# Performance work log

Hardware: AMD Instinct MI355X
Metric: run time of the kernel (lower is better)

Reference implementation:

```python
import jax, jax.numpy as jnp
import numpy as np

N, E, D, H = 100000, 1600000, 128, 4
HD = D // H  # per-head dim


def setup_inputs() -> dict:
    key = jax.random.key(0)
    ks = jax.random.split(key, 16)
    s = 1.0 / np.sqrt(D)
    inp = {
        "x": jax.random.normal(ks[0], (N, D), jnp.float32),
        "edge_index": jax.random.randint(ks[1], (2, E), 0, N, jnp.int64),
        # GCNConv params
        "w_gcn": jax.random.normal(ks[2], (D, D), jnp.float32) * s,
        "b_gcn": jnp.zeros((D,), jnp.float32),
        # TransformerConv params (lin_query/key/value, lin_skip, lin_beta)
        "w_q": jax.random.normal(ks[3], (D, D), jnp.float32) * s,
        "b_q": jnp.zeros((D,), jnp.float32),
        "w_k": jax.random.normal(ks[4], (D, D), jnp.float32) * s,
        "b_k": jnp.zeros((D,), jnp.float32),
        "w_v": jax.random.normal(ks[5], (D, D), jnp.float32) * s,
        "b_v": jnp.zeros((D,), jnp.float32),
        "w_skip": jax.random.normal(ks[6], (D, D), jnp.float32) * s,
        "b_skip": jnp.zeros((D,), jnp.float32),
        "w_beta": jax.random.normal(ks[7], (3 * D, 1), jnp.float32) * s,
        # LayerNorms
        "ln1_g": jnp.ones((D,), jnp.float32),
        "ln1_b": jnp.zeros((D,), jnp.float32),
        "ln2_g": jnp.ones((D,), jnp.float32),
        "ln2_b": jnp.zeros((D,), jnp.float32),
        # FFN
        "w1": jax.random.normal(ks[8], (D, 2 * D), jnp.float32) * s,
        "b1": jnp.zeros((2 * D,), jnp.float32),
        "w2": jax.random.normal(ks[9], (2 * D, D), jnp.float32) * (1.0 / np.sqrt(2 * D)),
        "b2": jnp.zeros((D,), jnp.float32),
        "local_weight": jnp.ones((1,), jnp.float32),
        "global_weight": jnp.ones((1,), jnp.float32),
    }
    return inp


def _layer_norm(x, g, b, eps=1e-5):
    mu = jnp.mean(x, axis=-1, keepdims=True)
    var = jnp.var(x, axis=-1, keepdims=True)
    return (x - mu) * jax.lax.rsqrt(var + eps) * g + b


def _gps_forward(x, edge_index, w_gcn, b_gcn, w_q, b_q, w_k, b_k, w_v, b_v,
                 w_skip, b_skip, w_beta, ln1_g, ln1_b, ln2_g, ln2_b,
                 w1, b1, w2, b2, local_weight, global_weight):
    src, dst = edge_index[0], edge_index[1]  # messages flow src -> dst

    # ---- GCNConv (add_self_loops=False), sym norm ----
    deg = jax.ops.segment_sum(jnp.ones((E,), x.dtype), dst, num_segments=N)
    dinv = jnp.where(deg > 0, jax.lax.rsqrt(jnp.maximum(deg, 1.0)), 0.0)
    norm = dinv[src] * dinv[dst]  # [E]
    h = x @ w_gcn  # [N, D]
    local_out = jax.ops.segment_sum(h[src] * norm[:, None], dst, num_segments=N) + b_gcn

    # ---- TransformerConv (heads=H, concat=True, beta=True) ----
    q = (x @ w_q + b_q).reshape(N, H, HD)
    k = (x @ w_k + b_k).reshape(N, H, HD)
    v = (x @ w_v + b_v).reshape(N, H, HD)
    scores = jnp.sum(q[dst] * k[src], axis=-1) / np.sqrt(HD)  # [E, H]
    m = jax.ops.segment_max(scores, dst, num_segments=N)      # [N, H]
    m = jnp.where(jnp.isfinite(m), m, 0.0)
    e = jnp.exp(scores - m[dst])                              # [E, H]
    denom = jax.ops.segment_sum(e, dst, num_segments=N)       # [N, H]
    alpha = e / denom[dst]                                    # [E, H]
    agg = jax.ops.segment_sum(v[src] * alpha[:, :, None], dst, num_segments=N)
    out_attn = agg.reshape(N, D)
    x_r = x @ w_skip + b_skip
    beta = jax.nn.sigmoid(
        jnp.concatenate([out_attn, x_r, out_attn - x_r], axis=-1) @ w_beta)  # [N,1]
    global_out = beta * x_r + (1.0 - beta) * out_attn

    # ---- combine + LN + FFN + LN ----
    xc = local_weight * local_out + global_weight * global_out
    xn = _layer_norm(xc + xc, ln1_g, ln1_b)
    ff = jnp.maximum(xn @ w1 + b1, 0.0) @ w2 + b2
    return _layer_norm(ff + xn, ln2_g, ln2_b)


def reference(x, edge_index, w_gcn, b_gcn, w_q, b_q, w_k, b_k, w_v, b_v,
              w_skip, b_skip, w_beta, ln1_g, ln1_b, ln2_g, ln2_b,
              w1, b1, w2, b2, local_weight, global_weight):
    return _gps_forward(x, edge_index, w_gcn, b_gcn, w_q, b_q, w_k, b_k, w_v, b_v,
                        w_skip, b_skip, w_beta, ln1_g, ln1_b, ln2_g, ln2_b,
                        w1, b1, w2, b2, local_weight, global_weight)
```

## Files before the change

kernel.cpp:

```cpp
#include <hip/hip_runtime.h>

typedef unsigned int u32;
typedef unsigned short u16;
typedef __attribute__((ext_vector_type(8))) short bf16x8;
typedef __attribute__((ext_vector_type(4))) float f32x4;

__device__ __forceinline__ float bf2f(u16 u){ return __uint_as_float(((u32)u) << 16); }
__device__ __forceinline__ float bf2f_lo(u32 u){ return __uint_as_float(u << 16); }
__device__ __forceinline__ float bf2f_hi(u32 u){ return __uint_as_float(u & 0xffff0000u); }
__device__ __forceinline__ u16 f2bf(float f){
  u32 x = __float_as_uint(f);
  return (u16)((x + 0x7fffu + ((x >> 16) & 1u)) >> 16);
}

__global__ void k_prep_all(const float* wq, const float* bq, const float* wsk, const float* bsk,
                           const float* wk, const float* bk, const float* wv, const float* bv,
                           const float* wg, const float* w1, const float* w2,
                           u16* WcatT, float* bcat, u16* w1T, u16* w2T){
  int idx = blockIdx.x * 256 + threadIdx.x;
  if (idx < 640 * 128){
    int col = idx >> 7, k = idx & 127;
    int blk = col >> 7, c = col & 127;
    const float* w = (blk==0)?wq:(blk==1)?wsk:(blk==2)?wk:(blk==3)?wv:wg;
    WcatT[idx] = f2bf(w[k * 128 + c]);
    if (k == 0){
      const float* b = (blk==0)?bq:(blk==1)?bsk:(blk==2)?bk:(blk==3)?bv:nullptr;
      bcat[col] = b ? b[c] : 0.0f;
    }
  } else if (idx < 640*128 + 256*128){
    int j = idx - 640*128; int c = j >> 7, k = j & 127;
    w1T[j] = f2bf(w1[k * 256 + c]);
  } else if (idx < 640*128 + 256*128 + 128*256){
    int j = idx - (640*128 + 256*128); int c = j >> 8, k = j & 255;
    w2T[j] = f2bf(w2[k * 128 + c]);
  }
}

__global__ void k_hist(const int* __restrict__ ei, int E, int* __restrict__ deg){
  int e = blockIdx.x * 256 + threadIdx.x;
  if (e >= E) return;
  atomicAdd(&deg[ei[E + e]], 1);
}
__global__ void k_scan_a(const int* __restrict__ deg, int N, int* __restrict__ bsum){
  __shared__ int sh[256];
  int b = blockIdx.x, t = threadIdx.x;
  int base = b * 1024 + t * 4, s = 0;
  #pragma unroll
  for (int j = 0; j < 4; j++){ int i = base + j; if (i < N) s += deg[i]; }
  sh[t] = s; __syncthreads();
  for (int off = 128; off > 0; off >>= 1){ if (t < off) sh[t] += sh[t + off]; __syncthreads(); }
  if (t == 0) bsum[b] = sh[0];
}
__global__ void k_scan_b(const int* __restrict__ bsum, int NB, int* __restrict__ boff){
  __shared__ int sh[1024];
  int t = threadIdx.x;
  int self = (t < NB) ? bsum[t] : 0;
  sh[t] = self; __syncthreads();
  for (int off = 1; off < 1024; off <<= 1){
    int v = sh[t]; int add = (t >= off) ? sh[t - off] : 0;
    __syncthreads(); sh[t] = v + add; __syncthreads();
  }
  if (t < NB) boff[t] = sh[t] - self;
}
__global__ void k_scan_c(const int* __restrict__ deg, int N, int E,
                         const int* __restrict__ boff, int* __restrict__ rowptr,
                         float* __restrict__ dinv){
  __shared__ int sh[256];
  int b = blockIdx.x, t = threadIdx.x;
  int base = b * 1024 + t * 4;
  int d[4]; int ts = 0;
  #pragma unroll
  for (int j = 0; j < 4; j++){ int i = base + j; d[j] = (i < N) ? deg[i] : 0; ts += d[j]; }
  sh[t] = ts; __syncthreads();
  for (int off = 1; off < 256; off <<= 1){
    int v = sh[t]; int add = (t >= off) ? sh[t - off] : 0;
    __syncthreads(); sh[t] = v + add; __syncthreads();
  }
  int excl = sh[t] - ts + boff[b];
  #pragma unroll
  for (int j = 0; j < 4; j++){
    int i = base + j;
    if (i < N){
      rowptr[i] = excl;
      dinv[i] = d[j] > 0 ? rsqrtf((float)d[j]) : 0.0f;
    }
    excl += d[j];
  }
  if (b == 0 && t == 0) rowptr[N] = E;
}
__global__ void k_csr(const int* __restrict__ ei, int E,
                      const int* __restrict__ rowptr, int* __restrict__ fill, int* __restrict__ csr){
  int e = blockIdx.x * 256 + threadIdx.x;
  if (e >= E) return;
  int d = ei[E + e];
  int pos = rowptr[d] + atomicAdd(&fill[d], 1);
  csr[pos] = ei[e];
}

__device__ __forceinline__ void stageTile(const u16* __restrict__ g, int ldg, int row0, int rclamp,
                                          int kofs, u16* lds){
  int t = threadIdx.x;
  #pragma unroll
  for (int p = 0; p < 8; p++){
    int chunk = p * 256 + t;
    int r = chunk >> 4;
    int cs = (chunk & 15) << 3;
    int rg = row0 + r; if (rg >= rclamp) rg = rclamp - 1;
    bf16x8 v = *(const bf16x8*)(g + (size_t)rg * ldg + kofs + cs);
    *(bf16x8*)(lds + r * 128 + (cs ^ ((r & 7) << 3))) = v;
  }
}
__device__ __forceinline__ void stageTileF32(const float* __restrict__ g, int ldg, int row0,
                                             int rclamp, u16* lds){
  int t = threadIdx.x;
  #pragma unroll
  for (int p = 0; p < 8; p++){
    int chunk = p * 256 + t;
    int r = chunk >> 4;
    int cs = (chunk & 15) << 3;
    int rg = row0 + r; if (rg >= rclamp) rg = rclamp - 1;
    const float* src = g + (size_t)rg * ldg + cs;
    float4 a = *(const float4*)(src);
    float4 b = *(const float4*)(src + 4);
    u16* dst = lds + r * 128 + (cs ^ ((r & 7) << 3));
    ushort4 lo; lo.x = f2bf(a.x); lo.y = f2bf(a.y); lo.z = f2bf(a.z); lo.w = f2bf(a.w);
    ushort4 hi; hi.x = f2bf(b.x); hi.y = f2bf(b.y); hi.z = f2bf(b.z); hi.w = f2bf(b.w);
    *(ushort4*)dst = lo;
    *(ushort4*)(dst + 4) = hi;
  }
}
__device__ __forceinline__ bf16x8 ldFrag(const u16* lds, int r, int k0){
  return *(const bf16x8*)(lds + r * 128 + (k0 ^ ((r & 7) << 3)));
}

__global__ __launch_bounds__(256) void k_gemm1(const float* __restrict__ x, const u16* __restrict__ WcatT,
    const float* __restrict__ bcat, u16* __restrict__ qB, u16* __restrict__ xrB,
    u16* __restrict__ kvhB, int N){
  __shared__ u16 As[128 * 128];
  __shared__ u16 Bs[128 * 128];
  int row0 = blockIdx.x * 128;
  stageTileF32(x, 128, row0, N, As);
  int t = threadIdx.x, l = t & 63, w = t >> 6;
  int wm = w >> 1, wn = w & 1;
  int c16 = l & 15, g = l >> 4;
  for (int cb = 0; cb < 5; cb++){
    stageTile(WcatT, 128, cb * 128, 1 << 30, 0, Bs);
    __syncthreads();
    f32x4 acc[4][4];
    #pragma unroll
    for (int mi = 0; mi < 4; mi++)
      #pragma unroll
      for (int ni = 0; ni < 4; ni++) acc[mi][ni] = (f32x4){0.f, 0.f, 0.f, 0.f};
    #pragma unroll
    for (int kk = 0; kk < 4; kk++){
      int k0 = kk * 32 + g * 8;
      bf16x8 af[4], bfr[4];
      #pragma unroll
      for (int mi = 0; mi < 4; mi++) af[mi] = ldFrag(As, wm * 64 + mi * 16 + c16, k0);
      #pragma unroll
      for (int ni = 0; ni < 4; ni++) bfr[ni] = ldFrag(Bs, wn * 64 + ni * 16 + c16, k0);
      #pragma unroll
      for (int mi = 0; mi < 4; mi++)
        #pragma unroll
        for (int ni = 0; ni < 4; ni++)
          acc[mi][ni] = __builtin_amdgcn_mfma_f32_16x16x32_bf16(af[mi], bfr[ni], acc[mi][ni], 0, 0, 0);
    }
    u16* dst; int ld, cofs;
    if (cb == 0){ dst = qB;  ld = 128; cofs = 0; }
    else if (cb == 1){ dst = xrB; ld = 128; cofs = 0; }
    else { dst = kvhB; ld = 384; cofs = (cb - 2) * 128; }
    float bias[4];
    #pragma unroll
    for (int ni = 0; ni < 4; ni++) bias[ni] = bcat[cb * 128 + wn * 64 + ni * 16 + c16];
    #pragma unroll
    for (int mi = 0; mi < 4; mi++){
      #pragma unroll
      for (int r = 0; r < 4; r++){
        int row = row0 + wm * 64 + mi * 16 + g * 4 + r;
        if (row < N){
          #pragma unroll
          for (int ni = 0; ni < 4; ni++)
            dst[(size_t)row * ld + cofs + wn * 64 + ni * 16 + c16] = f2bf(acc[mi][ni][r] + bias[ni]);
        }
      }
    }
    __syncthreads();
  }
}

__global__ __launch_bounds__(256) void k_edge(const u16* __restrict__ qB, const u16* __restrict__ xrB,
    const u16* __restrict__ kvhB,
    const int* __restrict__ csr, const int* __restrict__ rowptr, const float* __restrict__ dinv,
    const float* __restrict__ bgcn, const float* __restrict__ wbeta,
    const float* __restrict__ lng, const float* __restrict__ lnb,
    const float* __restrict__ lwp, const float* __restrict__ gwp,
    u16* __restrict__ xnB, int N){
  int lane = threadIdx.x & 63;
  int half = lane >> 5;
  int li = lane & 31;
  int d0 = li * 4;
  int n = blockIdx.x * 4 + (threadIdx.x >> 6);
  if (n >= N) return;
  int ro = rowptr[n], re = rowptr[n + 1];
  uint2 qu = *(const uint2*)(qB + (size_t)n * 128 + d0);
  float q0 = bf2f_lo(qu.x), q1 = bf2f_hi(qu.x), q2 = bf2f_lo(qu.y), q3 = bf2f_hi(qu.y);
  float av0 = 0, av1 = 0, av2 = 0, av3 = 0;
  float ah0 = 0, ah1 = 0, ah2 = 0, ah3 = 0;
  float den = 0;
  const float SC = 0.17677669529663687f;
  for (int e = ro + half; e < re; e += 2){
    int s = csr[e];
    const u16* fb = kvhB + (size_t)s * 384;
    uint2 ku = *(const uint2*)(fb + d0);
    uint2 vu = *(const uint2*)(fb + 128 + d0);
    uint2 hu = *(const uint2*)(fb + 256 + d0);
    float dv = dinv[s];
    float part = q0 * bf2f_lo(ku.x) + q1 * bf2f_hi(ku.x)
               + q2 * bf2f_lo(ku.y) + q3 * bf2f_hi(ku.y);
    part += __shfl_xor(part, 1);
    part += __shfl_xor(part, 2);
    part += __shfl_xor(part, 4);
    float p = __expf(part * SC);
    av0 += p * bf2f_lo(vu.x); av1 += p * bf2f_hi(vu.x);
    av2 += p * bf2f_lo(vu.y); av3 += p * bf2f_hi(vu.y);
    ah0 += dv * bf2f_lo(hu.x); ah1 += dv * bf2f_hi(hu.x);
    ah2 += dv * bf2f_lo(hu.y); ah3 += dv * bf2f_hi(hu.y);
    den += p;
  }
  den += __shfl_xor(den, 32);
  av0 += __shfl_xor(av0, 32); av1 += __shfl_xor(av1, 32);
  av2 += __shfl_xor(av2, 32); av3 += __shfl_xor(av3, 32);
  ah0 += __shfl_xor(ah0, 32); ah1 += __shfl_xor(ah1, 32);
  ah2 += __shfl_xor(ah2, 32); ah3 += __shfl_xor(ah3, 32);
  float inv_den = den > 0 ? 1.0f / den : 0.0f;
  float at0 = av0 * inv_den, at1 = av1 * inv_den, at2 = av2 * inv_den, at3 = av3 * inv_den;
  uint2 xru = *(const uint2*)(xrB + (size_t)n * 128 + d0);
  float xr0 = bf2f_lo(xru.x), xr1 = bf2f_hi(xru.x), xr2 = bf2f_lo(xru.y), xr3 = bf2f_hi(xru.y);
  float4 wb0 = *(const float4*)(wbeta + d0);
  float4 wb1 = *(const float4*)(wbeta + 128 + d0);
  float4 wb2 = *(const float4*)(wbeta + 256 + d0);
  float z = at0 * wb0.x + at1 * wb0.y + at2 * wb0.z + at3 * wb0.w
          + xr0 * wb1.x + xr1 * wb1.y + xr2 * wb1.z + xr3 * wb1.w
          + (at0 - xr0) * wb2.x + (at1 - xr1) * wb2.y
          + (at2 - xr2) * wb2.z + (at3 - xr3) * wb2.w;
  z += __shfl_xor(z, 1); z += __shfl_xor(z, 2); z += __shfl_xor(z, 4);
  z += __shfl_xor(z, 8); z += __shfl_xor(z, 16);
  float beta = 1.0f / (1.0f + __expf(-z));
  float dn = dinv[n];
  float4 bg = *(const float4*)(bgcn + d0);
  float l0 = dn * ah0 + bg.x, l1 = dn * ah1 + bg.y, l2 = dn * ah2 + bg.z, l3 = dn * ah3 + bg.w;
  float lw = lwp[0], gw = gwp[0];
  float ib = 1.0f - beta;
  float t0 = 2.0f * (lw * l0 + gw * (beta * xr0 + ib * at0));
  float t1 = 2.0f * (lw * l1 + gw * (beta * xr1 + ib * at1));
  float t2 = 2.0f * (lw * l2 + gw * (beta * xr2 + ib * at2));
  float t3 = 2.0f * (lw * l3 + gw * (beta * xr3 + ib * at3));
  float s = t0 + t1 + t2 + t3;
  float sq = t0*t0 + t1*t1 + t2*t2 + t3*t3;
  s += __shfl_xor(s, 1);  sq += __shfl_xor(sq, 1);
  s += __shfl_xor(s, 2);  sq += __shfl_xor(sq, 2);
  s += __shfl_xor(s, 4);  sq += __shfl_xor(sq, 4);
  s += __shfl_xor(s, 8);  sq += __shfl_xor(sq, 8);
  s += __shfl_xor(s, 16); sq += __shfl_xor(sq, 16);
  float mu = s * (1.0f / 128.0f);
  float var = sq * (1.0f / 128.0f) - mu * mu;
  float inv = rsqrtf(var + 1e-5f);
  if (half == 0){
    float4 gm = *(const float4*)(lng + d0);
    float4 bt = *(const float4*)(lnb + d0);
    float o0 = (t0 - mu) * inv * gm.x + bt.x;
    float o1 = (t1 - mu) * inv * gm.y + bt.y;
    float o2 = (t2 - mu) * inv * gm.z + bt.z;
    float o3 = (t3 - mu) * inv * gm.w + bt.w;
    uint2 pk;
    pk.x = (u32)f2bf(o0) | ((u32)f2bf(o1) << 16);
    pk.y = (u32)f2bf(o2) | ((u32)f2bf(o3) << 16);
    *(uint2*)(xnB + (size_t)n * 128 + d0) = pk;
  }
}

__global__ __launch_bounds__(256) void k_ffn1(const u16* __restrict__ xnB, const u16* __restrict__ w1T,
    const float* __restrict__ b1, u16* __restrict__ hid, int N){
  __shared__ u16 As[128 * 128];
  __shared__ u16 Bs[128 * 128];
  int row0 = blockIdx.x * 128, cb = blockIdx.y;
  stageTile(xnB, 128, row0, N, 0, As);
  stageTile(w1T, 128, cb * 128, 1 << 30, 0, Bs);
  __syncthreads();
  int t = threadIdx.x, l = t & 63, w = t >> 6;
  int wm = w >> 1, wn = w & 1;
  int c16 = l & 15, g = l >> 4;
  f32x4 acc[4][4];
  #pragma unroll
  for (int mi = 0; mi < 4; mi++)
    #pragma unroll
    for (int ni = 0; ni < 4; ni++) acc[mi][ni] = (f32x4){0.f, 0.f, 0.f, 0.f};
  #pragma unroll
  for (int kk = 0; kk < 4; kk++){
    int k0 = kk * 32 + g * 8;
    bf16x8 af[4], bfr[4];
    #pragma unroll
    for (int mi = 0; mi < 4; mi++) af[mi] = ldFrag(As, wm * 64 + mi * 16 + c16, k0);
    #pragma unroll
    for (int ni = 0; ni < 4; ni++) bfr[ni] = ldFrag(Bs, wn * 64 + ni * 16 + c16, k0);
    #pragma unroll
    for (int mi = 0; mi < 4; mi++)
      #pragma unroll
      for (int ni = 0; ni < 4; ni++)
        acc[mi][ni] = __builtin_amdgcn_mfma_f32_16x16x32_bf16(af[mi], bfr[ni], acc[mi][ni], 0, 0, 0);
  }
  float bias[4];
  #pragma unroll
  for (int ni = 0; ni < 4; ni++) bias[ni] = b1[cb * 128 + wn * 64 + ni * 16 + c16];
  #pragma unroll
  for (int mi = 0; mi < 4; mi++){
    #pragma unroll
    for (int r = 0; r < 4; r++){
      int row = row0 + wm * 64 + mi * 16 + g * 4 + r;
      if (row < N){
        #pragma unroll
        for (int ni = 0; ni < 4; ni++)
          hid[(size_t)row * 256 + cb * 128 + wn * 64 + ni * 16 + c16] =
              f2bf(fmaxf(acc[mi][ni][r] + bias[ni], 0.0f));
      }
    }
  }
}

__global__ __launch_bounds__(256) void k_ffn2(const u16* __restrict__ hid, const u16* __restrict__ w2T,
    const float* __restrict__ b2, const u16* __restrict__ xnB,
    const float* __restrict__ g2, const float* __restrict__ bt2,
    float* __restrict__ out, int N){
  __shared__ u16 As[128 * 128];
  __shared__ u16 Bs[128 * 128];
  int row0 = blockIdx.x * 128;
  int t = threadIdx.x, l = t & 63, w = t >> 6;
  int c16 = l & 15, g = l >> 4;
  f32x4 acc[2][8];
  #pragma unroll
  for (int mi = 0; mi < 2; mi++)
    #pragma unroll
    for (int ni = 0; ni < 8; ni++) acc[mi][ni] = (f32x4){0.f, 0.f, 0.f, 0.f};
  for (int kc = 0; kc < 2; kc++){
    if (kc) __syncthreads();
    stageTile(hid, 256, row0, N, kc * 128, As);
    stageTile(w2T, 256, 0, 1 << 30, kc * 128, Bs);
    __syncthreads();
    #pragma unroll
    for (int kk = 0; kk < 4; kk++){
      int k0 = kk * 32 + g * 8;
      bf16x8 af[2], bfr[8];
      #pragma unroll
      for (int mi = 0; mi < 2; mi++) af[mi] = ldFrag(As, w * 32 + mi * 16 + c16, k0);
      #pragma unroll
      for (int ni = 0; ni < 8; ni++) bfr[ni] = ldFrag(Bs, ni * 16 + c16, k0);
      #pragma unroll
      for (int mi = 0; mi < 2; mi++)
        #pragma unroll
        for (int ni = 0; ni < 8; ni++)
          acc[mi][ni] = __builtin_amdgcn_mfma_f32_16x16x32_bf16(af[mi], bfr[ni], acc[mi][ni], 0, 0, 0);
    }
  }
  float b2c[8], g2c[8], btc[8];
  #pragma unroll
  for (int ni = 0; ni < 8; ni++){
    int col = ni * 16 + c16;
    b2c[ni] = b2[col]; g2c[ni] = g2[col]; btc[ni] = bt2[col];
  }
  #pragma unroll
  for (int mi = 0; mi < 2; mi++){
    #pragma unroll
    for (int r = 0; r < 4; r++){
      int row = row0 + w * 32 + mi * 16 + g * 4 + r;
      int rc = row < N ? row : N - 1;
      float z[8]; float s = 0.f, sq = 0.f;
      #pragma unroll
      for (int ni = 0; ni < 8; ni++){
        float xv = bf2f(xnB[(size_t)rc * 128 + ni * 16 + c16]);
        z[ni] = acc[mi][ni][r] + b2c[ni] + xv;
        s += z[ni]; sq += z[ni] * z[ni];
      }
      s += __shfl_xor(s, 1); sq += __shfl_xor(sq, 1);
      s += __shfl_xor(s, 2); sq += __shfl_xor(sq, 2);
      s += __shfl_xor(s, 4); sq += __shfl_xor(sq, 4);
      s += __shfl_xor(s, 8); sq += __shfl_xor(sq, 8);
      float mu = s * (1.0f / 128.0f);
      float var = sq * (1.0f / 128.0f) - mu * mu;
      float inv = rsqrtf(var + 1e-5f);
      if (row < N){
        #pragma unroll
        for (int ni = 0; ni < 8; ni++)
          out[(size_t)row * 128 + ni * 16 + c16] = (z[ni] - mu) * inv * g2c[ni] + btc[ni];
      }
    }
  }
}

extern "C" void kernel_launch(void* const* d_in, const int* in_sizes, int n_in,
                              void* d_out, int out_size, void* d_ws, size_t ws_size,
                              hipStream_t stream){
  const float* x      = (const float*)d_in[0];
  const int*   ei     = (const int*)d_in[1];
  const float* w_gcn  = (const float*)d_in[2];
  const float* b_gcn  = (const float*)d_in[3];
  const float* w_q    = (const float*)d_in[4];
  const float* b_q    = (const float*)d_in[5];
  const float* w_k    = (const float*)d_in[6];
  const float* b_k    = (const float*)d_in[7];
  const float* w_v    = (const float*)d_in[8];
  const float* b_v    = (const float*)d_in[9];
  const float* w_skip = (const float*)d_in[10];
  const float* b_skip = (const float*)d_in[11];
  const float* w_beta = (const float*)d_in[12];
  const float* ln1_g  = (const float*)d_in[13];
  const float* ln1_b  = (const float*)d_in[14];
  const float* ln2_g  = (const float*)d_in[15];
  const float* ln2_b  = (const float*)d_in[16];
  const float* w1     = (const float*)d_in[17];
  const float* b1     = (const float*)d_in[18];
  const float* w2     = (const float*)d_in[19];
  const float* b2     = (const float*)d_in[20];
  const float* lw     = (const float*)d_in[21];
  const float* gw     = (const float*)d_in[22];
  int N = in_sizes[0] / 128;
  int E = in_sizes[1] / 2;
  float* outf = (float*)d_out;

  char* ws = (char*)d_ws;
  size_t off = 0;
  auto alloc = [&](size_t bytes) -> char* {
    char* p = ws + off; off += (bytes + 255) & ~(size_t)255; return p;
  };
  u16* kvhB   = (u16*)alloc((size_t)N * 384 * 2);
  u16* xrB    = (u16*)alloc((size_t)N * 128 * 2);
  u16* qB     = (u16*)alloc((size_t)N * 128 * 2);
  u16* xnB    = (u16*)alloc((size_t)N * 128 * 2);
  int* csr    = (int*)alloc((size_t)E * 4);
  int* deg    = (int*)alloc((size_t)N * 4);
  int* rowptr = (int*)alloc((size_t)(N + 1) * 4);
  int* fill   = (int*)alloc((size_t)N * 4);
  float* dinv = (float*)alloc((size_t)N * 4);
  int NB = (N + 1023) >> 10;
  int* bsum   = (int*)alloc((size_t)NB * 4);
  int* boff   = (int*)alloc((size_t)NB * 4);
  u16* WcatT  = (u16*)alloc((size_t)640 * 128 * 2);
  float* bcat = (float*)alloc((size_t)640 * 4);
  u16* w1T    = (u16*)alloc((size_t)256 * 128 * 2);
  u16* w2T    = (u16*)alloc((size_t)128 * 256 * 2);
  u16* hid    = kvhB;

  if (off > ws_size) return;

  hipMemsetAsync(deg, 0, (size_t)N * 4, stream);
  hipMemsetAsync(fill, 0, (size_t)N * 4, stream);

  k_prep_all<<<576, 256, 0, stream>>>(w_q, b_q, w_skip, b_skip, w_k, b_k, w_v, b_v, w_gcn,
                                      w1, w2, WcatT, bcat, w1T, w2T);
  k_hist<<<(E + 255) / 256, 256, 0, stream>>>(ei, E, deg);
  k_scan_a<<<NB, 256, 0, stream>>>(deg, N, bsum);
  k_scan_b<<<1, 1024, 0, stream>>>(bsum, NB, boff);
  k_scan_c<<<NB, 256, 0, stream>>>(deg, N, E, boff, rowptr, dinv);
  k_csr<<<(E + 255) / 256, 256, 0, stream>>>(ei, E, rowptr, fill, csr);

  int MB = (N + 127) / 128;
  k_gemm1<<<MB, 256, 0, stream>>>(x, WcatT, bcat, qB, xrB, kvhB, N);
  k_edge<<<(N + 3) / 4, 256, 0, stream>>>(qB, xrB, kvhB, csr, rowptr, dinv, b_gcn, w_beta,
                                          ln1_g, ln1_b, lw, gw, xnB, N);
  dim3 f1(MB, 2);
  k_ffn1<<<f1, 256, 0, stream>>>(xnB, w1T, b1, hid, N);
  k_ffn2<<<MB, 256, 0, stream>>>(hid, w2T, b2, xnB, ln2_g, ln2_b, outf, N);
}
```

Baseline: 455.3 us.

## Fuse FFN kernels via LDS hidden tile, prescale GCN features by dinv, reuse deg for CSR fill

Merges the two FFN GEMM kernels into one that keeps the 64x256 ReLU hidden tile in shared memory, so the hidden activations no longer make a round trip through global memory. The GCN source-side dinv scaling moves into the first GEMM epilogue, which removes a per-edge dinv gather in the edge kernel. CSR construction now decrements the degree array instead of incrementing a separate zeroed fill array, dropping one memset and one buffer. The fused FFN uses 64 KB of LDS per block with smaller row tiles, which may lower occupancy and reload the weights once per 64 rows.

```diff
diff --git a/kernel.cpp b/kernel.cpp
--- a/kernel.cpp
+++ b/kernel.cpp
@@ -89,11 +89,11 @@
   if (b == 0 && t == 0) rowptr[N] = E;
 }
 __global__ void k_csr(const int* __restrict__ ei, int E,
-                      const int* __restrict__ rowptr, int* __restrict__ fill, int* __restrict__ csr){
+                      const int* __restrict__ rowptr, int* __restrict__ deg, int* __restrict__ csr){
   int e = blockIdx.x * 256 + threadIdx.x;
   if (e >= E) return;
   int d = ei[E + e];
-  int pos = rowptr[d] + atomicAdd(&fill[d], 1);
+  int pos = rowptr[d] + atomicSub(&deg[d], 1) - 1;
   csr[pos] = ei[e];
 }
 
@@ -134,8 +134,8 @@
 }
 
 __global__ __launch_bounds__(256) void k_gemm1(const float* __restrict__ x, const u16* __restrict__ WcatT,
-    const float* __restrict__ bcat, u16* __restrict__ qB, u16* __restrict__ xrB,
-    u16* __restrict__ kvhB, int N){
+    const float* __restrict__ bcat, const float* __restrict__ dinv,
+    u16* __restrict__ qB, u16* __restrict__ xrB, u16* __restrict__ kvhB, int N){
   __shared__ u16 As[128 * 128];
   __shared__ u16 Bs[128 * 128];
   int row0 = blockIdx.x * 128;
@@ -165,10 +165,6 @@
         for (int ni = 0; ni < 4; ni++)
           acc[mi][ni] = __builtin_amdgcn_mfma_f32_16x16x32_bf16(af[mi], bfr[ni], acc[mi][ni], 0, 0, 0);
     }
-    u16* dst; int ld, cofs;
-    if (cb == 0){ dst = qB;  ld = 128; cofs = 0; }
-    else if (cb == 1){ dst = xrB; ld = 128; cofs = 0; }
-    else { dst = kvhB; ld = 384; cofs = (cb - 2) * 128; }
     float bias[4];
     #pragma unroll
     for (int ni = 0; ni < 4; ni++) bias[ni] = bcat[cb * 128 + wn * 64 + ni * 16 + c16];
@@ -178,9 +174,23 @@
       for (int r = 0; r < 4; r++){
         int row = row0 + wm * 64 + mi * 16 + g * 4 + r;
         if (row < N){
-          #pragma unroll
-          for (int ni = 0; ni < 4; ni++)
-            dst[(size_t)row * ld + cofs + wn * 64 + ni * 16 + c16] = f2bf(acc[mi][ni][r] + bias[ni]);
+          if (cb == 0 || cb == 1){
+            u16* dst = (cb == 0 ? qB : xrB) + (size_t)row * 128;
+            #pragma unroll
+            for (int ni = 0; ni < 4; ni++)
+              dst[wn * 64 + ni * 16 + c16] = f2bf(acc[mi][ni][r] + bias[ni]);
+          } else if (cb == 4){
+            float dv = dinv[row];
+            u16* dst = kvhB + (size_t)row * 384 + 256;
+            #pragma unroll
+            for (int ni = 0; ni < 4; ni++)
+              dst[wn * 64 + ni * 16 + c16] = f2bf(acc[mi][ni][r] * dv);
+          } else {
+            u16* dst = kvhB + (size_t)row * 384 + (cb - 2) * 128;
+            #pragma unroll
+            for (int ni = 0; ni < 4; ni++)
+              dst[wn * 64 + ni * 16 + c16] = f2bf(acc[mi][ni][r] + bias[ni]);
+          }
         }
       }
     }
@@ -214,7 +224,6 @@
     uint2 ku = *(const uint2*)(fb + d0);
     uint2 vu = *(const uint2*)(fb + 128 + d0);
     uint2 hu = *(const uint2*)(fb + 256 + d0);
-    float dv = dinv[s];
     float part = q0 * bf2f_lo(ku.x) + q1 * bf2f_hi(ku.x)
                + q2 * bf2f_lo(ku.y) + q3 * bf2f_hi(ku.y);
     part += __shfl_xor(part, 1);
@@ -223,8 +232,8 @@
     float p = __expf(part * SC);
     av0 += p * bf2f_lo(vu.x); av1 += p * bf2f_hi(vu.x);
     av2 += p * bf2f_lo(vu.y); av3 += p * bf2f_hi(vu.y);
-    ah0 += dv * bf2f_lo(hu.x); ah1 += dv * bf2f_hi(hu.x);
-    ah2 += dv * bf2f_lo(hu.y); ah3 += dv * bf2f_hi(hu.y);
+    ah0 += bf2f_lo(hu.x); ah1 += bf2f_hi(hu.x);
+    ah2 += bf2f_lo(hu.y); ah3 += bf2f_hi(hu.y);
     den += p;
   }
   den += __shfl_xor(den, 32);
@@ -279,87 +288,86 @@
   }
 }
 
-__global__ __launch_bounds__(256) void k_ffn1(const u16* __restrict__ xnB, const u16* __restrict__ w1T,
-    const float* __restrict__ b1, u16* __restrict__ hid, int N){
-  __shared__ u16 As[128 * 128];
-  __shared__ u16 Bs[128 * 128];
-  int row0 = blockIdx.x * 128, cb = blockIdx.y;
-  stageTile(xnB, 128, row0, N, 0, As);
-  stageTile(w1T, 128, cb * 128, 1 << 30, 0, Bs);
-  __syncthreads();
-  int t = threadIdx.x, l = t & 63, w = t >> 6;
-  int wm = w >> 1, wn = w & 1;
-  int c16 = l & 15, g = l >> 4;
-  f32x4 acc[4][4];
-  #pragma unroll
-  for (int mi = 0; mi < 4; mi++)
-    #pragma unroll
-    for (int ni = 0; ni < 4; ni++) acc[mi][ni] = (f32x4){0.f, 0.f, 0.f, 0.f};
-  #pragma unroll
-  for (int kk = 0; kk < 4; kk++){
-    int k0 = kk * 32 + g * 8;
-    bf16x8 af[4], bfr[4];
-    #pragma unroll
-    for (int mi = 0; mi < 4; mi++) af[mi] = ldFrag(As, wm * 64 + mi * 16 + c16, k0);
-    #pragma unroll
-    for (int ni = 0; ni < 4; ni++) bfr[ni] = ldFrag(Bs, wn * 64 + ni * 16 + c16, k0);
-    #pragma unroll
-    for (int mi = 0; mi < 4; mi++)
-      #pragma unroll
-      for (int ni = 0; ni < 4; ni++)
-        acc[mi][ni] = __builtin_amdgcn_mfma_f32_16x16x32_bf16(af[mi], bfr[ni], acc[mi][ni], 0, 0, 0);
-  }
-  float bias[4];
-  #pragma unroll
-  for (int ni = 0; ni < 4; ni++) bias[ni] = b1[cb * 128 + wn * 64 + ni * 16 + c16];
-  #pragma unroll
-  for (int mi = 0; mi < 4; mi++){
-    #pragma unroll
-    for (int r = 0; r < 4; r++){
-      int row = row0 + wm * 64 + mi * 16 + g * 4 + r;
-      if (row < N){
-        #pragma unroll
-        for (int ni = 0; ni < 4; ni++)
-          hid[(size_t)row * 256 + cb * 128 + wn * 64 + ni * 16 + c16] =
-              f2bf(fmaxf(acc[mi][ni][r] + bias[ni], 0.0f));
-      }
-    }
-  }
-}
-
-__global__ __launch_bounds__(256) void k_ffn2(const u16* __restrict__ hid, const u16* __restrict__ w2T,
-    const float* __restrict__ b2, const u16* __restrict__ xnB,
+__global__ __launch_bounds__(256) void k_ffn(const u16* __restrict__ xnB, const u16* __restrict__ w1T,
+    const float* __restrict__ b1, const u16* __restrict__ w2T, const float* __restrict__ b2,
     const float* __restrict__ g2, const float* __restrict__ bt2,
     float* __restrict__ out, int N){
-  __shared__ u16 As[128 * 128];
-  __shared__ u16 Bs[128 * 128];
-  int row0 = blockIdx.x * 128;
+  __shared__ u16 L[32768];
+  int row0 = blockIdx.x * 64;
   int t = threadIdx.x, l = t & 63, w = t >> 6;
   int c16 = l & 15, g = l >> 4;
-  f32x4 acc[2][8];
-  #pragma unroll
-  for (int mi = 0; mi < 2; mi++)
-    #pragma unroll
-    for (int ni = 0; ni < 8; ni++) acc[mi][ni] = (f32x4){0.f, 0.f, 0.f, 0.f};
-  for (int kc = 0; kc < 2; kc++){
-    if (kc) __syncthreads();
-    stageTile(hid, 256, row0, N, kc * 128, As);
-    stageTile(w2T, 256, 0, 1 << 30, kc * 128, Bs);
+  #pragma unroll
+  for (int p = 0; p < 4; p++){
+    int chunk = p * 256 + t;
+    int r = chunk >> 4, cs = (chunk & 15) << 3;
+    int rg = row0 + r; if (rg >= N) rg = N - 1;
+    bf16x8 v = *(const bf16x8*)(xnB + (size_t)rg * 128 + cs);
+    *(bf16x8*)(L + r * 128 + (cs ^ ((r & 7) << 3))) = v;
+  }
+  f32x4 acc1[2][8];
+  #pragma unroll
+  for (int cb = 0; cb < 2; cb++)
+    #pragma unroll
+    for (int ni = 0; ni < 8; ni++) acc1[cb][ni] = (f32x4){0.f, 0.f, 0.f, 0.f};
+  for (int cb = 0; cb < 2; cb++){
+    #pragma unroll
+    for (int p = 0; p < 8; p++){
+      int chunk = p * 256 + t;
+      int r = chunk >> 4, cs = (chunk & 15) << 3;
+      bf16x8 v = *(const bf16x8*)(w1T + (size_t)(cb * 128 + r) * 128 + cs);
+      *(bf16x8*)(L + 8192 + r * 128 + (cs ^ ((r & 7) << 3))) = v;
+    }
     __syncthreads();
     #pragma unroll
     for (int kk = 0; kk < 4; kk++){
       int k0 = kk * 32 + g * 8;
-      bf16x8 af[2], bfr[8];
-      #pragma unroll
-      for (int mi = 0; mi < 2; mi++) af[mi] = ldFrag(As, w * 32 + mi * 16 + c16, k0);
-      #pragma unroll
-      for (int ni = 0; ni < 8; ni++) bfr[ni] = ldFrag(Bs, ni * 16 + c16, k0);
-      #pragma unroll
-      for (int mi = 0; mi < 2; mi++)
-        #pragma unroll
-        for (int ni = 0; ni < 8; ni++)
-          acc[mi][ni] = __builtin_amdgcn_mfma_f32_16x16x32_bf16(af[mi], bfr[ni], acc[mi][ni], 0, 0, 0);
-    }
+      bf16x8 af = ldFrag(L, w * 16 + c16, k0);
+      #pragma unroll
+      for (int ni = 0; ni < 8; ni++){
+        bf16x8 bfr = ldFrag(L + 8192, ni * 16 + c16, k0);
+        acc1[cb][ni] = __builtin_amdgcn_mfma_f32_16x16x32_bf16(af, bfr, acc1[cb][ni], 0, 0, 0);
+      }
+    }
+    __syncthreads();
+  }
+  #pragma unroll
+  for (int cb = 0; cb < 2; cb++){
+    #pragma unroll
+    for (int ni = 0; ni < 8; ni++){
+      float bias = b1[cb * 128 + ni * 16 + c16];
+      #pragma unroll
+      for (int r = 0; r < 4; r++){
+        int rl = w * 16 + g * 4 + r;
+        int col = cb * 128 + ni * 16 + c16;
+        L[rl * 256 + (col ^ ((rl & 7) << 3))] = f2bf(fmaxf(acc1[cb][ni][r] + bias, 0.f));
+      }
+    }
+  }
+  __syncthreads();
+  f32x4 acc2[8];
+  #pragma unroll
+  for (int ni = 0; ni < 8; ni++) acc2[ni] = (f32x4){0.f, 0.f, 0.f, 0.f};
+  for (int kc = 0; kc < 2; kc++){
+    #pragma unroll
+    for (int p = 0; p < 8; p++){
+      int chunk = p * 256 + t;
+      int r = chunk >> 4, cs = (chunk & 15) << 3;
+      bf16x8 v = *(const bf16x8*)(w2T + (size_t)r * 256 + kc * 128 + cs);
+      *(bf16x8*)(L + 16384 + r * 128 + (cs ^ ((r & 7) << 3))) = v;
+    }
+    __syncthreads();
+    #pragma unroll
+    for (int kk = 0; kk < 4; kk++){
+      int k0 = kk * 32 + g * 8;
+      int rowl = w * 16 + c16;
+      bf16x8 af = *(const bf16x8*)(L + rowl * 256 + ((kc * 128 + k0) ^ ((rowl & 7) << 3)));
+      #pragma unroll
+      for (int ni = 0; ni < 8; ni++){
+        bf16x8 bfr = ldFrag(L + 16384, ni * 16 + c16, k0);
+        acc2[ni] = __builtin_amdgcn_mfma_f32_16x16x32_bf16(af, bfr, acc2[ni], 0, 0, 0);
+      }
+    }
+    __syncthreads();
   }
   float b2c[8], g2c[8], btc[8];
   #pragma unroll
@@ -368,30 +376,27 @@
     b2c[ni] = b2[col]; g2c[ni] = g2[col]; btc[ni] = bt2[col];
   }
   #pragma unroll
-  for (int mi = 0; mi < 2; mi++){
-    #pragma unroll
-    for (int r = 0; r < 4; r++){
-      int row = row0 + w * 32 + mi * 16 + g * 4 + r;
-      int rc = row < N ? row : N - 1;
-      float z[8]; float s = 0.f, sq = 0.f;
-      #pragma unroll
-      for (int ni = 0; ni < 8; ni++){
-        float xv = bf2f(xnB[(size_t)rc * 128 + ni * 16 + c16]);
-        z[ni] = acc[mi][ni][r] + b2c[ni] + xv;
-        s += z[ni]; sq += z[ni] * z[ni];
-      }
-      s += __shfl_xor(s, 1); sq += __shfl_xor(sq, 1);
-      s += __shfl_xor(s, 2); sq += __shfl_xor(sq, 2);
-      s += __shfl_xor(s, 4); sq += __shfl_xor(sq, 4);
-      s += __shfl_xor(s, 8); sq += __shfl_xor(sq, 8);
-      float mu = s * (1.0f / 128.0f);
-      float var = sq * (1.0f / 128.0f) - mu * mu;
-      float inv = rsqrtf(var + 1e-5f);
-      if (row < N){
-        #pragma unroll
-        for (int ni = 0; ni < 8; ni++)
-          out[(size_t)row * 128 + ni * 16 + c16] = (z[ni] - mu) * inv * g2c[ni] + btc[ni];
-      }
+  for (int r = 0; r < 4; r++){
+    int row = row0 + w * 16 + g * 4 + r;
+    int rc = row < N ? row : N - 1;
+    float z[8]; float s = 0.f, sq = 0.f;
+    #pragma unroll
+    for (int ni = 0; ni < 8; ni++){
+      float xv = bf2f(xnB[(size_t)rc * 128 + ni * 16 + c16]);
+      z[ni] = acc2[ni][r] + b2c[ni] + xv;
+      s += z[ni]; sq += z[ni] * z[ni];
+    }
+    s += __shfl_xor(s, 1); sq += __shfl_xor(sq, 1);
+    s += __shfl_xor(s, 2); sq += __shfl_xor(sq, 2);
+    s += __shfl_xor(s, 4); sq += __shfl_xor(sq, 4);
+    s += __shfl_xor(s, 8); sq += __shfl_xor(sq, 8);
+    float mu = s * (1.0f / 128.0f);
+    float var = sq * (1.0f / 128.0f) - mu * mu;
+    float inv = rsqrtf(var + 1e-5f);
+    if (row < N){
+      #pragma unroll
+      for (int ni = 0; ni < 8; ni++)
+        out[(size_t)row * 128 + ni * 16 + c16] = (z[ni] - mu) * inv * g2c[ni] + btc[ni];
     }
   }
 }
@@ -438,7 +443,6 @@
   int* csr    = (int*)alloc((size_t)E * 4);
   int* deg    = (int*)alloc((size_t)N * 4);
   int* rowptr = (int*)alloc((size_t)(N + 1) * 4);
-  int* fill   = (int*)alloc((size_t)N * 4);
   float* dinv = (float*)alloc((size_t)N * 4);
   int NB = (N + 1023) >> 10;
   int* bsum   = (int*)alloc((size_t)NB * 4);
@@ -447,12 +451,10 @@
   float* bcat = (float*)alloc((size_t)640 * 4);
   u16* w1T    = (u16*)alloc((size_t)256 * 128 * 2);
   u16* w2T    = (u16*)alloc((size_t)128 * 256 * 2);
-  u16* hid    = kvhB;
 
   if (off > ws_size) return;
 
   hipMemsetAsync(deg, 0, (size_t)N * 4, stream);
-  hipMemsetAsync(fill, 0, (size_t)N * 4, stream);
 
   k_prep_all<<<576, 256, 0, stream>>>(w_q, b_q, w_skip, b_skip, w_k, b_k, w_v, b_v, w_gcn,
                                       w1, w2, WcatT, bcat, w1T, w2T);
@@ -460,13 +462,12 @@
   k_scan_a<<<NB, 256, 0, stream>>>(deg, N, bsum);
   k_scan_b<<<1, 1024, 0, stream>>>(bsum, NB, boff);
   k_scan_c<<<NB, 256, 0, stream>>>(deg, N, E, boff, rowptr, dinv);
-  k_csr<<<(E + 255) / 256, 256, 0, stream>>>(ei, E, rowptr, fill, csr);
+  k_csr<<<(E + 255) / 256, 256, 0, stream>>>(ei, E, rowptr, deg, csr);
 
   int MB = (N + 127) / 128;
-  k_gemm1<<<MB, 256, 0, stream>>>(x, WcatT, bcat, qB, xrB, kvhB, N);
+  k_gemm1<<<MB, 256, 0, stream>>>(x, WcatT, bcat, dinv, qB, xrB, kvhB, N);
   k_edge<<<(N + 3) / 4, 256, 0, stream>>>(qB, xrB, kvhB, csr, rowptr, dinv, b_gcn, w_beta,
                                           ln1_g, ln1_b, lw, gw, xnB, N);
-  dim3 f1(MB, 2);
-  k_ffn1<<<f1, 256, 0, stream>>>(xnB, w1T, b1, hid, N);
-  k_ffn2<<<MB, 256, 0, stream>>>(hid, w2T, b2, xnB, ln2_g, ln2_b, outf, N);
-}
+  int MB64 = (N + 63) / 64;
+  k_ffn<<<MB64, 256, 0, stream>>>(xnB, w1T, b1, w2T, b2, ln2_g, ln2_b, outf, N);
+}
```

New measurement: 443.2 us. -2.7%, faster.
